# Performance work log

Hardware: AMD Instinct MI355X
Metric: run time of the kernel (lower is better)

## Reference

```python
import jax, jax.numpy as jnp
import numpy as np
from jax.scipy.special import logsumexp

B, L = 32, 128
NEG = -1e9
SPAN_LAMB = 0.5


def setup_inputs() -> dict:
    key = jax.random.key(0)
    ks = jax.random.split(key, 8)
    span_logits = jax.random.normal(ks[0], (B, L, L, 2), jnp.float32)
    ph = jax.random.normal(ks[1], (B, L, L), jnp.float32)
    pt = jax.random.normal(ks[2], (B, L, L), jnp.float32)
    ph_arc = jax.random.normal(ks[3], (B, L, L), jnp.float32)
    spans_ind = jax.random.randint(ks[4], (B, L, L), 0, 3, jnp.int32)
    ph_ind = jax.random.randint(ks[5], (B, L, L), 0, 2, jnp.int32)
    pt_ind = jax.random.randint(ks[6], (B, L, L), 0, 2, jnp.int32)
    lens = jax.random.randint(ks[7], (B,), L // 2, L + 1, jnp.int32)
    i = jnp.arange(L)
    # maskspan[b,i,j] = valid right-closed span i..j within sentence b; row 0 sums to lens
    maskspan = (i[None, :, None] <= i[None, None, :]) & (i[None, None, :] < lens[:, None, None])
    maskarc = (i[None, :, None] < lens[:, None, None]) & (i[None, None, :] < lens[:, None, None])
    return dict(span_logits=span_logits, ph=ph, pt=pt, ph_arc=ph_arc,
                spans_ind=spans_ind, ph_ind=ph_ind, pt_ind=pt_ind,
                maskspan=maskspan, maskarc=maskarc)


def _inside_logZ(span_logits, lens):
    # CYK inside algorithm over right-closed spans; returns sum_b logZ_b.
    scores = logsumexp(span_logits, axis=-1)  # [B,L,L] span score = lse over labels
    Ln = scores.shape[1]
    ar = jnp.arange(Ln)
    # width-0 base: s[i,i] = scores[i,i]
    s0 = jnp.where(jnp.eye(Ln, dtype=bool)[None], scores, NEG)
    li = ar[:, None] + ar[None, :]        # [L,L]: left child right end i+k
    ri = li + 1                           # right child left end i+k+1
    li_c = jnp.clip(li, 0, Ln - 1)
    ri_c = jnp.clip(ri, 0, Ln - 1)

    def step(s, w):
        j = ar + w
        jc = jnp.clip(j, 0, Ln - 1)
        left = s[:, ar[:, None], li_c]                 # [B,L,L] left[b,i,k]=s[b,i,i+k]
        right = s[:, ri_c, jc[:, None]]                # right[b,i,k]=s[b,i+k+1,i+w]
        comb = jnp.where(ar[None, None, :] < w, left + right, NEG)
        new = scores[:, ar, jc] + logsumexp(comb, axis=-1)  # [B,L]
        valid = (j < Ln)[None, :]
        cur = s[:, ar, jc]
        s = s.at[:, ar, jc].set(jnp.where(valid, new, cur))
        return s, None

    s, _ = jax.lax.scan(step, s0, jnp.arange(1, Ln))
    logZ = jnp.take_along_axis(s[:, 0, :], (lens - 1)[:, None], axis=1)[:, 0]
    return logZ.sum()


def _bce_mean(x, y, m):
    # stable BCEWithLogits, mean over masked elements
    l = jnp.maximum(x, 0.0) - x * y + jnp.log1p(jnp.exp(-jnp.abs(x)))
    return jnp.where(m, l, 0.0).sum() / m.sum().astype(jnp.float32)


def reference(span_logits, ph, pt, ph_arc, spans_ind, ph_ind, pt_ind, maskspan, maskarc):
    lens = maskspan[:, 0].sum(-1)                         # [B]
    spans_b = jnp.where(spans_ind > 0, spans_ind - 1, spans_ind).astype(bool)
    # label marginals = d logZ / d span_logits (matches torch autograd-based cyk)
    marginals = jax.grad(_inside_logZ)(span_logits, lens)  # [B,L,L,2]
    pos_mask = maskspan & spans_b
    neg_mask = maskspan & (~spans_b)
    pos_loss = jnp.log(jnp.where(pos_mask, jnp.maximum(marginals[..., 1], 1e-38), 1.0)).sum()
    neg_loss = jnp.log(jnp.where(neg_mask, jnp.maximum(marginals[..., 0], 1e-38), 1.0)).sum()
    loss_spans = -(pos_loss + neg_loss) / lens.sum().astype(jnp.float32)
    loss_ph = _bce_mean(ph, ph_ind.astype(jnp.float32), maskarc)
    loss_pt = _bce_mean(pt, pt_ind.astype(jnp.float32), maskarc)
    return SPAN_LAMB * loss_spans + (1.0 - SPAN_LAMB) * (loss_ph + loss_pt)
```

## Files before the change

kernel.cpp:

```cpp
#include <hip/hip_runtime.h>
#include <float.h>

#define NB 32
#define NBCE 32
#define L 128
#define NT 1024
#define R 132
#define PAD 8
#define LOGMIN -87.49823f

__device__ __forceinline__ int mask_mode(const void* p) {
    unsigned int v = ((const unsigned int*)p)[0];
    if (v == 1u) return 1;
    if (v == 0x3F800000u) return 2;
    return 0;
}
__device__ __forceinline__ bool mask_at(const void* p, int mode, int idx) {
    if (mode == 1) return ((const int*)p)[idx] != 0;
    if (mode == 2) return ((const float*)p)[idx] != 0.0f;
    return ((const unsigned char*)p)[idx] != 0;
}

__device__ __forceinline__ float lse2(float a, float b) {
    return fmaxf(a, b) + log1pf(__expf(-fabsf(a - b)));
}

template<int C>
__device__ __forceinline__ float dppf(float x) {
    return __int_as_float(__builtin_amdgcn_mov_dpp(__float_as_int(x), C, 0xF, 0xF, true));
}
template<int T>
__device__ __forceinline__ float bfly_max(float x) {
    x = fmaxf(x, dppf<0xB1>(x));
    x = fmaxf(x, dppf<0x4E>(x));
    x = fmaxf(x, dppf<0x141>(x));
    if (T == 16) x = fmaxf(x, dppf<0x140>(x));
    return x;
}
template<int T>
__device__ __forceinline__ float bfly_add(float x) {
    x += dppf<0xB1>(x);
    x += dppf<0x4E>(x);
    x += dppf<0x141>(x);
    if (T == 16) x += dppf<0x140>(x);
    return x;
}

template<int T, int M>
__device__ __forceinline__ void load_blk(float4* buf, int sub, int clo, int chi,
                                         const float* p1, const float* p2, float& mloc) {
    const int kb0 = clo >> 2;
#pragma unroll
    for (int m = 0; m < M; ++m) {
        const int c0 = (kb0 + sub + T * m) << 2;
        if (c0 >= chi) break;
        const float4 a = *(const float4*)(p1 + c0);
        const float4 b = *(const float4*)(p2 + c0);
        const unsigned rng = (unsigned)(chi - clo);
        float4 v;
        v.x = ((unsigned)(c0 + 0 - clo) < rng) ? a.x + b.x : -FLT_MAX;
        v.y = ((unsigned)(c0 + 1 - clo) < rng) ? a.y + b.y : -FLT_MAX;
        v.z = ((unsigned)(c0 + 2 - clo) < rng) ? a.z + b.z : -FLT_MAX;
        v.w = ((unsigned)(c0 + 3 - clo) < rng) ? a.w + b.w : -FLT_MAX;
        buf[m] = v;
        mloc = fmaxf(mloc, fmaxf(fmaxf(v.x, v.y), fmaxf(v.z, v.w)));
    }
}
template<int T, int M>
__device__ __forceinline__ void sumexp_blk(const float4* buf, int sub, int clo, int chi,
                                           float Mv, float& s) {
    const int kb0 = clo >> 2;
#pragma unroll
    for (int m = 0; m < M; ++m) {
        const int c0 = (kb0 + sub + T * m) << 2;
        if (c0 >= chi) break;
        const float4 v = buf[m];
        s += __expf(v.x - Mv) + __expf(v.y - Mv) + __expf(v.z - Mv) + __expf(v.w - Mv);
    }
}

__global__ __launch_bounds__(NT, 1) void tree_dp_kernel(
    const float* __restrict__ logits,
    const int*   __restrict__ spans_ind,
    const void*  __restrict__ maskspan,
    const float* __restrict__ ph, const float* __restrict__ pt,
    const int* __restrict__ ph_ind, const int* __restrict__ pt_ind,
    const void* __restrict__ maskarc,
    double*      __restrict__ ws)
{
    const int tid = threadIdx.x;

    if (blockIdx.x >= NB) {
        const int mode = mask_mode(maskarc);
        const int tot = NB * L * L;
        double sph = 0.0, spt = 0.0, cnt = 0.0;
        for (int idx = (blockIdx.x - NB) * NT + tid; idx < tot; idx += NBCE * NT) {
            if (mask_at(maskarc, mode, idx)) {
                float x = ph[idx]; float y = (float)ph_ind[idx];
                sph += (double)(fmaxf(x, 0.0f) - x * y + log1pf(__expf(-fabsf(x))));
                x = pt[idx]; y = (float)pt_ind[idx];
                spt += (double)(fmaxf(x, 0.0f) - x * y + log1pf(__expf(-fabsf(x))));
                cnt += 1.0;
            }
        }
        for (int off = 32; off > 0; off >>= 1) {
            sph += __shfl_down(sph, off);
            spt += __shfl_down(spt, off);
            cnt += __shfl_down(cnt, off);
        }
        if ((tid & 63) == 0) {
            atomicAdd(&ws[2], sph); atomicAdd(&ws[3], spt); atomicAdd(&ws[4], cnt);
        }
        return;
    }

    __shared__ __align__(16) float Am[L * R + PAD];
    __shared__ __align__(16) float Gm[L * R + PAD];

    const int b = blockIdx.x;
    const int mbase = b * L * L;
    const int mode = mask_mode(maskspan);

    int predv = (tid < L) && mask_at(maskspan, mode, mbase + tid);
    const int n = __syncthreads_count(predv);

    const float* lg = logits + (size_t)b * L * L * 2;
    const int* si = spans_ind + mbase;

    for (int e = tid; e < L * L; e += NT) {
        int ii = e >> 7, jj = e & (L - 1);
        if (ii <= jj && jj < n) {
            const float* p = lg + (size_t)e * 2;
            float v = lse2(p[0], p[1]);
            Am[ii * R + jj] = v;
            if (ii >= 1) Am[jj * R + ii - 1] = v;
            Gm[ii * R + jj] = v; Gm[jj * R + ii] = v;
        }
    }
    __syncthreads();

    for (int w = 1; w < n; ++w) {
        const int c = n - w;
        if (c > 64) {
            const int cell = tid >> 3, sub = tid & 7;
            if (cell < c) {
                const int i = cell, j = i + w;
                float4 buf[3]; float mloc = -FLT_MAX;
                load_blk<8, 3>(buf, sub, i, j, &Am[i * R], &Am[j * R], mloc);
                float Mv = bfly_max<8>(mloc);
                float s = 0.0f;
                sumexp_blk<8, 3>(buf, sub, i, j, Mv, s);
                float S = bfly_add<8>(s);
                if (sub == 0) {
                    float val = Am[i * R + j] + Mv + __logf(S);
                    Am[i * R + j] = val;
                    Am[j * R + i - 1] = val;
                }
            }
        } else {
            const int cell = tid >> 4, sub = tid & 15;
            if (cell < c) {
                const int i = cell, j = i + w;
                float4 buf[2]; float mloc = -FLT_MAX;
                load_blk<16, 2>(buf, sub, i, j, &Am[i * R], &Am[j * R], mloc);
                float Mv = bfly_max<16>(mloc);
                float s = 0.0f;
                sumexp_blk<16, 2>(buf, sub, i, j, Mv, s);
                float S = bfly_add<16>(s);
                if (sub == 0) {
                    float val = Am[i * R + j] + Mv + __logf(S);
                    Am[i * R + j] = val;
                    Am[j * R + i - 1] = val;
                }
            }
        }
        __syncthreads();
    }

    const float logZ = Am[n - 1];

    {
        float tmp[16];
#pragma unroll
        for (int p = 0; p < 16; ++p) {
            const int e = tid + p * NT;
            const int r = e >> 7, cc = e & (L - 1);
            tmp[p] = 0.0f;
            if (cc < r && r < n)
                tmp[p] = (cc == 0) ? Am[r] : Am[r * R + cc - 1];
        }
        __syncthreads();
#pragma unroll
        for (int p = 0; p < 16; ++p) {
            const int e = tid + p * NT;
            const int r = e >> 7, cc = e & (L - 1);
            if (cc < r && r < n) Am[r * R + cc] = tmp[p];
        }
    }
    __syncthreads();

    for (int w = n - 2; w >= 1; --w) {
        const int c = n - w;
        if (c > 64) {
            const int cell = tid >> 3, sub = tid & 7;
            if (cell < c) {
                const int i = cell, j = i + w;
                float4 b1[4], b2[4]; float mloc = -FLT_MAX;
                load_blk<8, 4>(b1, sub, j + 1, n, &Gm[i * R], &Am[(j + 1) * R], mloc);
                const float* pa2 = &Am[(i >= 1 ? i - 1 : 0) * R];
                load_blk<8, 4>(b2, sub, 0, i, &Gm[j * R], pa2, mloc);
                float Mv = bfly_max<8>(mloc);
                float s = 0.0f;
                sumexp_blk<8, 4>(b1, sub, j + 1, n, Mv, s);
                sumexp_blk<8, 4>(b2, sub, 0, i, Mv, s);
                float S = bfly_add<8>(s);
                if (sub == 0) {
                    float val = Gm[i * R + j] + Mv + __logf(S);
                    Gm[i * R + j] = val; Gm[j * R + i] = val;
                }
            }
        } else {
            const int cell = tid >> 4, sub = tid & 15;
            if (cell < c) {
                const int i = cell, j = i + w;
                float4 b1[2], b2[1]; float mloc = -FLT_MAX;
                load_blk<16, 2>(b1, sub, j + 1, n, &Gm[i * R], &Am[(j + 1) * R], mloc);
                const float* pa2 = &Am[(i >= 1 ? i - 1 : 0) * R];
                load_blk<16, 1>(b2, sub, 0, i, &Gm[j * R], pa2, mloc);
                float Mv = bfly_max<16>(mloc);
                float s = 0.0f;
                sumexp_blk<16, 2>(b1, sub, j + 1, n, Mv, s);
                sumexp_blk<16, 1>(b2, sub, 0, i, Mv, s);
                float S = bfly_add<16>(s);
                if (sub == 0) {
                    float val = Gm[i * R + j] + Mv + __logf(S);
                    Gm[i * R + j] = val; Gm[j * R + i] = val;
                }
            }
        }
        __syncthreads();
    }

    double local = 0.0;
    {
        const int cell = tid >> 3, sub = tid & 7;
        if (cell < n) {
            const int i = cell;
            float4 b1[4], b2[4]; float mloc = -FLT_MAX;
            const float* pa1 = &Am[(i + 1 < n ? i + 1 : 0) * R];
            load_blk<8, 4>(b1, sub, i + 1, n, &Gm[i * R], pa1, mloc);
            const float* pa2 = &Am[(i >= 1 ? i - 1 : 0) * R];
            load_blk<8, 4>(b2, sub, 0, i, &Gm[i * R], pa2, mloc);
            float Mv = bfly_max<8>(mloc);
            float s = 0.0f;
            sumexp_blk<8, 4>(b1, sub, i + 1, n, Mv, s);
            sumexp_blk<8, 4>(b2, sub, 0, i, Mv, s);
            float S = bfly_add<8>(s);
            if (sub == 0) {
                float beta_ii = Mv + __logf(S);
                const float* p = lg + ((size_t)i * L + i) * 2;
                float lc = (si[i * L + i] == 2) ? p[1] : p[0];
                local += (double)fmaxf(beta_ii - logZ + lc, LOGMIN);
            }
        }
    }

    for (int e = tid; e < L * L; e += NT) {
        int ii = e >> 7, jj = e & (L - 1);
        if (ii < jj && jj < n) {
            const float* p = lg + (size_t)e * 2;
            float a = p[0], cc = p[1];
            float sc = lse2(a, cc);
            float lc = (si[e] == 2) ? cc : a;
            float logm = Am[ii * R + jj] + Gm[ii * R + jj] - logZ + lc - 2.0f * sc;
            local += (double)fmaxf(logm, LOGMIN);
        }
    }

    for (int off = 32; off > 0; off >>= 1)
        local += __shfl_down(local, off);
    if ((tid & 63) == 0) atomicAdd(&ws[0], local);
    if (tid == 0) atomicAdd(&ws[1], (double)n);
}

__global__ void finalize_kernel(const double* __restrict__ ws, float* __restrict__ out) {
    double loss_spans = -ws[0] / ws[1];
    double bce = (ws[2] + ws[3]) / ws[4];
    out[0] = (float)(0.5 * loss_spans + 0.5 * bce);
}

extern "C" void kernel_launch(void* const* d_in, const int* in_sizes, int n_in,
                              void* d_out, int out_size, void* d_ws, size_t ws_size,
                              hipStream_t stream) {
    (void)in_sizes; (void)n_in; (void)out_size; (void)ws_size;
    const float* span_logits = (const float*)d_in[0];
    const float* ph          = (const float*)d_in[1];
    const float* pt          = (const float*)d_in[2];
    const int*   spans_ind   = (const int*)d_in[4];
    const int*   ph_ind      = (const int*)d_in[5];
    const int*   pt_ind      = (const int*)d_in[6];
    const void*  maskspan    = d_in[7];
    const void*  maskarc     = d_in[8];
    double* ws = (double*)d_ws;
    float* out = (float*)d_out;

    hipMemsetAsync(d_ws, 0, 5 * sizeof(double), stream);
    hipLaunchKernelGGL(tree_dp_kernel, dim3(NB + NBCE), dim3(NT), 0, stream,
                       span_logits, spans_ind, maskspan,
                       ph, pt, ph_ind, pt_ind, maskarc, ws);
    hipLaunchKernelGGL(finalize_kernel, dim3(1), dim3(1), 0, stream, ws, out);
}
```

Measured before the change: 343.6 us.

## Block inside/outside CYK passes into 8-width chunks with register-level wavefront updates

Replaces the one-barrier-per-width inside and outside DP loops with chunks of eight widths. Each chunk first computes a bulk partial logsumexp (max, sum) for every cell from already-finished spans, cooperatively across the block into a shared P buffer. Three wavefronts then finish the dependent in-chunk terms in registers, using shuffles and online-merge logsumexp. This cuts the number of __syncthreads by roughly 8x and removes the 16-thread-per-cell path, at the cost of much more intricate index logic and extra per-chunk serial work on three wavefronts.

```diff
diff --git a/kernel.cpp b/kernel.cpp
--- a/kernel.cpp
+++ b/kernel.cpp
@@ -29,20 +29,16 @@
 __device__ __forceinline__ float dppf(float x) {
     return __int_as_float(__builtin_amdgcn_mov_dpp(__float_as_int(x), C, 0xF, 0xF, true));
 }
-template<int T>
-__device__ __forceinline__ float bfly_max(float x) {
+__device__ __forceinline__ float bfly_max8(float x) {
     x = fmaxf(x, dppf<0xB1>(x));
     x = fmaxf(x, dppf<0x4E>(x));
     x = fmaxf(x, dppf<0x141>(x));
-    if (T == 16) x = fmaxf(x, dppf<0x140>(x));
     return x;
 }
-template<int T>
-__device__ __forceinline__ float bfly_add(float x) {
+__device__ __forceinline__ float bfly_add8(float x) {
     x += dppf<0xB1>(x);
     x += dppf<0x4E>(x);
     x += dppf<0x141>(x);
-    if (T == 16) x += dppf<0x140>(x);
     return x;
 }
 
@@ -79,6 +75,18 @@
     }
 }
 
+__device__ __forceinline__ void omerge(float t, float& m, float& s) {
+    float nm = fmaxf(m, t);
+    s = s * __expf(m - nm) + __expf(t - nm);
+    m = nm;
+}
+__device__ __forceinline__ void omerge_mask(float t, bool mk, float& m, float& s) {
+    float tm = mk ? t : -FLT_MAX;
+    float nm = fmaxf(m, tm);
+    s = s * __expf(m - nm) + (mk ? __expf(t - nm) : 0.0f);
+    m = nm;
+}
+
 __global__ __launch_bounds__(NT, 1) void tree_dp_kernel(
     const float* __restrict__ logits,
     const int*   __restrict__ spans_ind,
@@ -116,6 +124,7 @@
 
     __shared__ __align__(16) float Am[L * R + PAD];
     __shared__ __align__(16) float Gm[L * R + PAD];
+    __shared__ float2 P[8][128];
 
     const int b = blockIdx.x;
     const int mbase = b * L * L;
@@ -139,38 +148,97 @@
     }
     __syncthreads();
 
-    for (int w = 1; w < n; ++w) {
-        const int c = n - w;
-        if (c > 64) {
-            const int cell = tid >> 3, sub = tid & 7;
-            if (cell < c) {
-                const int i = cell, j = i + w;
-                float4 buf[3]; float mloc = -FLT_MAX;
-                load_blk<8, 3>(buf, sub, i, j, &Am[i * R], &Am[j * R], mloc);
-                float Mv = bfly_max<8>(mloc);
-                float s = 0.0f;
-                sumexp_blk<8, 3>(buf, sub, i, j, Mv, s);
-                float S = bfly_add<8>(s);
-                if (sub == 0) {
-                    float val = Am[i * R + j] + Mv + __logf(S);
-                    Am[i * R + j] = val;
-                    Am[j * R + i - 1] = val;
-                }
-            }
-        } else {
-            const int cell = tid >> 4, sub = tid & 15;
-            if (cell < c) {
-                const int i = cell, j = i + w;
-                float4 buf[2]; float mloc = -FLT_MAX;
-                load_blk<16, 2>(buf, sub, i, j, &Am[i * R], &Am[j * R], mloc);
-                float Mv = bfly_max<16>(mloc);
-                float s = 0.0f;
-                sumexp_blk<16, 2>(buf, sub, i, j, Mv, s);
-                float S = bfly_add<16>(s);
-                if (sub == 0) {
-                    float val = Am[i * R + j] + Mv + __logf(S);
-                    Am[i * R + j] = val;
-                    Am[j * R + i - 1] = val;
+    const int wv = tid >> 6;
+    const int ln = tid & 63;
+    const int bcell = wv * 56 + ln;
+    const int ic = min(bcell, L - 1);
+    const bool ownIn  = (wv < 2) ? (ln < 56) : (ln < 16);
+    const bool ownOut = (wv == 0) ? true : (ln >= 8 && ln < ((wv == 1) ? 64 : 16));
+    float llo[7];
+    float vlo[8];
+
+    if (wv < 3) {
+        float r[8];
+        const float ld0 = Am[ic * R + ic];
+#pragma unroll
+        for (int d = 0; d < 8; ++d) {
+            const int w = d + 1;
+            const bool valid = (bcell + w < n);
+            const int jcl = min(bcell + w, L - 1);
+            const float dsc = Am[jcl * R + jcl];
+            const float scij = Gm[ic * R + jcl];
+            float m = -FLT_MAX, s = 0.0f;
+#pragma unroll
+            for (int e = 0; e < 8; ++e) {
+                if (e < w) {
+                    const int f = w - 1 - e;
+                    float lv = (e == 0) ? ld0 : r[e - 1];
+                    float rv = (f == 0) ? dsc : __shfl_down(r[f - 1], e + 1);
+                    omerge(lv + rv, m, s);
+                }
+            }
+            float val = scij + m + __logf(s);
+            r[d] = val;
+            if (valid && ownIn) {
+                Am[bcell * R + bcell + w] = val;
+                Am[(bcell + w) * R + bcell - 1] = val;
+            }
+        }
+        llo[0] = ld0;
+#pragma unroll
+        for (int e = 1; e < 7; ++e)
+            llo[e] = r[e - 1];
+    }
+    __syncthreads();
+
+    for (int w0 = 9; w0 < n; w0 += 8) {
+        {
+            const int cellA = tid >> 3, sub = tid & 7;
+#pragma unroll
+            for (int d = 0; d < 8; ++d) {
+                const int w = w0 + d;
+                if (w < n && cellA < n - w) {
+                    const int i = cellA, j = i + w;
+                    float4 buf[4]; float mloc = -FLT_MAX;
+                    load_blk<8, 4>(buf, sub, i + d, i + w0, &Am[i * R], &Am[j * R], mloc);
+                    float Mv = bfly_max8(mloc);
+                    float s = 0.0f;
+                    sumexp_blk<8, 4>(buf, sub, i + d, i + w0, Mv, s);
+                    float S = bfly_add8(s);
+                    if (sub == 0) P[d][i] = make_float2(Mv, S);
+                }
+            }
+        }
+        __syncthreads();
+        if (wv < 3) {
+            float r[8];
+#pragma unroll
+            for (int d = 0; d < 8; ++d) {
+                const int w = w0 + d;
+                const bool valid = (w < n) && (bcell + w < n);
+                const int jcl = min(bcell + w, L - 1);
+                float2 pp = P[d][ic];
+                float m = pp.x, s = pp.y;
+#pragma unroll
+                for (int e = 0; e < 7; ++e) {
+                    if (e < d) {
+                        float rv = __shfl_down(r[d - 1 - e], e + 1);
+                        omerge(llo[e] + rv, m, s);
+                    }
+                }
+#pragma unroll
+                for (int h = 0; h < 7; ++h) {
+                    if (h < d) {
+                        float rv = Am[jcl * R + min(ic + w0 + h, L - 1)];
+                        omerge(r[h] + rv, m, s);
+                    }
+                }
+                float scij = Gm[ic * R + jcl];
+                float val = scij + m + __logf(s);
+                r[d] = val;
+                if (valid && ownIn) {
+                    Am[bcell * R + bcell + w] = val;
+                    Am[(bcell + w) * R + bcell - 1] = val;
                 }
             }
         }
@@ -184,57 +252,99 @@
 #pragma unroll
         for (int p = 0; p < 16; ++p) {
             const int e = tid + p * NT;
-            const int r = e >> 7, cc = e & (L - 1);
+            const int rr = e >> 7, cc = e & (L - 1);
             tmp[p] = 0.0f;
-            if (cc < r && r < n)
-                tmp[p] = (cc == 0) ? Am[r] : Am[r * R + cc - 1];
+            if (cc < rr && rr < n)
+                tmp[p] = (cc == 0) ? Am[rr] : Am[rr * R + cc - 1];
         }
         __syncthreads();
 #pragma unroll
         for (int p = 0; p < 16; ++p) {
             const int e = tid + p * NT;
-            const int r = e >> 7, cc = e & (L - 1);
-            if (cc < r && r < n) Am[r * R + cc] = tmp[p];
+            const int rr = e >> 7, cc = e & (L - 1);
+            if (cc < rr && rr < n) Am[rr * R + cc] = tmp[p];
         }
     }
     __syncthreads();
 
-    for (int w = n - 2; w >= 1; --w) {
-        const int c = n - w;
-        if (c > 64) {
-            const int cell = tid >> 3, sub = tid & 7;
-            if (cell < c) {
-                const int i = cell, j = i + w;
-                float4 b1[4], b2[4]; float mloc = -FLT_MAX;
-                load_blk<8, 4>(b1, sub, j + 1, n, &Gm[i * R], &Am[(j + 1) * R], mloc);
-                const float* pa2 = &Am[(i >= 1 ? i - 1 : 0) * R];
-                load_blk<8, 4>(b2, sub, 0, i, &Gm[j * R], pa2, mloc);
-                float Mv = bfly_max<8>(mloc);
-                float s = 0.0f;
-                sumexp_blk<8, 4>(b1, sub, j + 1, n, Mv, s);
-                sumexp_blk<8, 4>(b2, sub, 0, i, Mv, s);
-                float S = bfly_add<8>(s);
-                if (sub == 0) {
-                    float val = Gm[i * R + j] + Mv + __logf(S);
-                    Gm[i * R + j] = val; Gm[j * R + i] = val;
-                }
-            }
-        } else {
-            const int cell = tid >> 4, sub = tid & 15;
-            if (cell < c) {
-                const int i = cell, j = i + w;
-                float4 b1[2], b2[1]; float mloc = -FLT_MAX;
-                load_blk<16, 2>(b1, sub, j + 1, n, &Gm[i * R], &Am[(j + 1) * R], mloc);
-                const float* pa2 = &Am[(i >= 1 ? i - 1 : 0) * R];
-                load_blk<16, 1>(b2, sub, 0, i, &Gm[j * R], pa2, mloc);
-                float Mv = bfly_max<16>(mloc);
-                float s = 0.0f;
-                sumexp_blk<16, 2>(b1, sub, j + 1, n, Mv, s);
-                sumexp_blk<16, 1>(b2, sub, 0, i, Mv, s);
-                float S = bfly_add<16>(s);
-                if (sub == 0) {
-                    float val = Gm[i * R + j] + Mv + __logf(S);
-                    Gm[i * R + j] = val; Gm[j * R + i] = val;
+    if (wv < 3) {
+        const int im1 = max(ic - 1, 0);
+#pragma unroll
+        for (int v = 1; v < 8; ++v)
+            vlo[v] = Am[im1 * R + max(ic - v, 0)];
+    }
+
+    const int bTop = 1 + 8 * ((n - 3) >> 3);
+    for (int b0 = bTop; b0 >= 1; b0 -= 8) {
+        float scg[8];
+        if (wv < 3) {
+#pragma unroll
+            for (int d = 0; d < 8; ++d)
+                scg[d] = Gm[ic * R + min(ic + b0 + d, L - 1)];
+        }
+        {
+            const int cellA = tid >> 3, sub = tid & 7;
+#pragma unroll
+            for (int d = 0; d < 8; ++d) {
+                const int w = b0 + d;
+                if (w <= n - 2 && cellA < n - w) {
+                    const int i = cellA, j = i + w;
+                    float mloc = -FLT_MAX;
+                    float4 b1[4], b2[4];
+                    const int clo1 = j + (8 - d);
+                    const bool h1 = clo1 < n;
+                    if (h1) load_blk<8, 4>(b1, sub, clo1, n, &Gm[i * R], &Am[(j + 1) * R], mloc);
+                    const int chi2 = i + d - 7;
+                    const bool h2 = chi2 > 0;
+                    if (h2) load_blk<8, 4>(b2, sub, 0, chi2, &Gm[j * R], &Am[(i - 1) * R], mloc);
+                    float Mv = bfly_max8(mloc);
+                    float s = 0.0f;
+                    if (h1) sumexp_blk<8, 4>(b1, sub, clo1, n, Mv, s);
+                    if (h2) sumexp_blk<8, 4>(b2, sub, 0, chi2, Mv, s);
+                    float S = bfly_add8(s);
+                    if (sub == 0) P[d][i] = make_float2(Mv, S);
+                }
+            }
+        }
+        __syncthreads();
+        if (wv < 3) {
+            float r[8];
+#pragma unroll
+            for (int dd = 0; dd < 8; ++dd) {
+                const int d = 7 - dd;
+                const int w = b0 + d;
+                const bool valid = (w <= n - 2) && (bcell + w < n);
+                const int j = bcell + w;
+                const int jcl = min(j, L - 1);
+                const int jp1 = min(j + 1, L - 1);
+                float2 pp = P[d][ic];
+                float m = pp.x, s = pp.y;
+#pragma unroll
+                for (int u = 1; u < 8; ++u) {
+                    if (u < 8 - d) {
+                        const bool mk = valid && (j + u < n);
+                        float g = (w + u < n - 1) ? r[d + u] : Gm[ic * R + min(j + u, L - 1)];
+                        float a = Am[jp1 * R + min(j + u, L - 1)];
+                        omerge_mask(g + a, mk, m, s);
+                    }
+                }
+#pragma unroll
+                for (int v = 1; v < 8; ++v) {
+                    if (v < 8 - d) {
+                        float g;
+                        if (w + v < n - 1)
+                            g = __shfl_up(r[d + v], v);
+                        else
+                            g = Gm[jcl * R + max(bcell - v, 0)];
+                        const bool mk = valid && (bcell - v >= 0);
+                        omerge_mask(g + vlo[v], mk, m, s);
+                    }
+                }
+                float val = scg[d] + m + __logf(s);
+                r[d] = val;
+                if (valid && ownOut) {
+                    Gm[bcell * R + j] = val;
+                    Gm[j * R + bcell] = val;
                 }
             }
         }
@@ -250,12 +360,12 @@
             const float* pa1 = &Am[(i + 1 < n ? i + 1 : 0) * R];
             load_blk<8, 4>(b1, sub, i + 1, n, &Gm[i * R], pa1, mloc);
             const float* pa2 = &Am[(i >= 1 ? i - 1 : 0) * R];
-            load_blk<8, 4>(b2, sub, 0, i, &Gm[i * R], pa2, mloc);
-            float Mv = bfly_max<8>(mloc);
+            if (i > 0) load_blk<8, 4>(b2, sub, 0, i, &Gm[i * R], pa2, mloc);
+            float Mv = bfly_max8(mloc);
             float s = 0.0f;
             sumexp_blk<8, 4>(b1, sub, i + 1, n, Mv, s);
-            sumexp_blk<8, 4>(b2, sub, 0, i, Mv, s);
-            float S = bfly_add<8>(s);
+            if (i > 0) sumexp_blk<8, 4>(b2, sub, 0, i, Mv, s);
+            float S = bfly_add8(s);
             if (sub == 0) {
                 float beta_ii = Mv + __logf(S);
                 const float* p = lg + ((size_t)i * L + i) * 2;
```

Measured after the change: 420.0 us. 22.2% more time.

## Process two DP diagonals per barrier using wave shuffles and LDS flags

Applied to the files above, without the earlier changes.

The inside and outside CYK sweeps now handle two span widths per __syncthreads. The second width's log-sum-exp is computed from the terms already available and then merged online with the two terms that depend on the first width. Those neighbour values come through wave shuffles, or through a workgroup-scope acquire/release flag spin-wait when the neighbour cell sits in another wavefront. Storage also changes: Am is kept symmetric instead of shifted, loads switch from float4 to scalar strided reads, and the padding grows. The aim is to halve the number of block-wide barriers on the serial critical path, at the cost of spin-waits, scalar LDS loads and a more complex dependency scheme.

```diff
diff --git a/kernel.cpp b/kernel.cpp
--- a/kernel.cpp
+++ b/kernel.cpp
@@ -6,7 +6,7 @@
 #define L 128
 #define NT 1024
 #define R 132
-#define PAD 8
+#define PAD 40
 #define LOGMIN -87.49823f
 
 __device__ __forceinline__ int mask_mode(const void* p) {
@@ -46,36 +46,153 @@
     return x;
 }
 
-template<int T, int M>
-__device__ __forceinline__ void load_blk(float4* buf, int sub, int clo, int chi,
-                                         const float* p1, const float* p2, float& mloc) {
-    const int kb0 = clo >> 2;
+template<int T, int NU>
+__device__ __forceinline__ void load_terms(float* v, int sub, int nterm,
+                                           const float* p1, const float* p2, float& mloc) {
+    p1 += sub; p2 += sub;
 #pragma unroll
-    for (int m = 0; m < M; ++m) {
-        const int c0 = (kb0 + sub + T * m) << 2;
-        if (c0 >= chi) break;
-        const float4 a = *(const float4*)(p1 + c0);
-        const float4 b = *(const float4*)(p2 + c0);
-        const unsigned rng = (unsigned)(chi - clo);
-        float4 v;
-        v.x = ((unsigned)(c0 + 0 - clo) < rng) ? a.x + b.x : -FLT_MAX;
-        v.y = ((unsigned)(c0 + 1 - clo) < rng) ? a.y + b.y : -FLT_MAX;
-        v.z = ((unsigned)(c0 + 2 - clo) < rng) ? a.z + b.z : -FLT_MAX;
-        v.w = ((unsigned)(c0 + 3 - clo) < rng) ? a.w + b.w : -FLT_MAX;
-        buf[m] = v;
-        mloc = fmaxf(mloc, fmaxf(fmaxf(v.x, v.y), fmaxf(v.z, v.w)));
-    }
-}
-template<int T, int M>
-__device__ __forceinline__ void sumexp_blk(const float4* buf, int sub, int clo, int chi,
-                                           float Mv, float& s) {
-    const int kb0 = clo >> 2;
+    for (int m = 0; m < NU; ++m) {
+        if (m * T >= nterm) break;
+        float a = p1[m * T] + p2[m * T];
+        a = (sub + m * T < nterm) ? a : -FLT_MAX;
+        v[m] = a;
+        mloc = fmaxf(mloc, a);
+    }
+}
+template<int T, int NU>
+__device__ __forceinline__ void sum_exp(const float* v, int nterm, float M, float& s) {
 #pragma unroll
-    for (int m = 0; m < M; ++m) {
-        const int c0 = (kb0 + sub + T * m) << 2;
-        if (c0 >= chi) break;
-        const float4 v = buf[m];
-        s += __expf(v.x - Mv) + __expf(v.y - Mv) + __expf(v.z - Mv) + __expf(v.w - Mv);
+    for (int m = 0; m < NU; ++m) {
+        if (m * T >= nterm) break;
+        s += __expf(v[m] - M);
+    }
+}
+
+template<int T, int NU>
+__device__ __forceinline__ void lse_part1(const float* p1, const float* p2, int nt,
+                                          int sub, float& M, float& S) {
+    float v[NU]; float mloc = -FLT_MAX;
+    load_terms<T, NU>(v, sub, nt, p1, p2, mloc);
+    float Mv = bfly_max<T>(mloc);
+    float s = 0.0f;
+    sum_exp<T, NU>(v, nt, Mv, s);
+    S = bfly_add<T>(s);
+    M = Mv;
+}
+template<int T, int NU1, int NU2>
+__device__ __forceinline__ void lse_part2(const float* a1, const float* a2, int nt1,
+                                          const float* b1, const float* b2, int nt2,
+                                          int sub, float& M, float& S) {
+    float v1[NU1]; float v2[NU2]; float mloc = -FLT_MAX;
+    load_terms<T, NU1>(v1, sub, nt1, a1, a2, mloc);
+    load_terms<T, NU2>(v2, sub, nt2, b1, b2, mloc);
+    float Mv = bfly_max<T>(mloc);
+    float s = 0.0f;
+    sum_exp<T, NU1>(v1, nt1, Mv, s);
+    sum_exp<T, NU2>(v2, nt2, Mv, s);
+    S = bfly_add<T>(s);
+    M = Mv;
+}
+
+__device__ __forceinline__ void omerge(float t, float& m, float& s) {
+    float nm = fmaxf(m, t);
+    s = s * __expf(m - nm) + __expf(t - nm);
+    m = nm;
+}
+__device__ __forceinline__ void omerge_mask(float t, bool mk, float& m, float& s) {
+    float tm = mk ? t : -FLT_MAX;
+    float nm = fmaxf(m, tm);
+    s = s * __expf(m - nm) + (mk ? __expf(t - nm) : 0.0f);
+    m = nm;
+}
+
+__device__ __forceinline__ void pub(int* f, int ep) {
+    __hip_atomic_store(f, ep, __ATOMIC_RELEASE, __HIP_MEMORY_SCOPE_WORKGROUP);
+}
+__device__ __forceinline__ void waitflag(int* f, int ep) {
+    while (__hip_atomic_load(f, __ATOMIC_ACQUIRE, __HIP_MEMORY_SCOPE_WORKGROUP) < ep) {}
+}
+
+template<int T>
+__device__ __forceinline__ void inside_pair(float* Am, int* flag, int n, int w, int tid) {
+    const int i = tid / T, sub = tid % T;
+    const int c = n - w;
+    const int j = i + w, j2 = j + 1;
+    const bool act1 = (i < c);
+    const bool act2 = (w + 1 < n) && (i < c - 1);
+    float val1 = -FLT_MAX;
+    if (act1) {
+        float M, S;
+        lse_part1<T, 8>(&Am[i * R + i], &Am[j * R + i + 1], w, sub, M, S);
+        val1 = Am[i * R + j] + M + __logf(S);
+        if (sub == 0) {
+            Am[i * R + j] = val1;
+            Am[j * R + i] = val1;
+            pub(&flag[i], w);
+        }
+    }
+    float M2 = -FLT_MAX, S2 = 0.0f;
+    if (act2)
+        lse_part1<T, 8>(&Am[i * R + i + 1], &Am[j2 * R + i + 2], w - 1, sub, M2, S2);
+    float sh = __shfl_down(val1, T);
+    if (act2) {
+        float nb;
+        if ((i & (64 / T - 1)) == (64 / T - 1)) {
+            waitflag(&flag[i + 1], w);
+            nb = Am[(i + 1) * R + j2];
+        } else nb = sh;
+        float m = M2, s = S2;
+        omerge(val1 + Am[j2 * R + j2], m, s);
+        omerge(Am[i * R + i] + nb, m, s);
+        float val2 = Am[i * R + j2] + m + __logf(s);
+        if (sub == 0) { Am[i * R + j2] = val2; Am[j2 * R + i] = val2; }
+    }
+}
+
+template<int T, int NU>
+__device__ __forceinline__ void outside_pair(const float* Am, float* Gm, int* flag,
+                                             int n, int w, int ep, int tid) {
+    const int i = tid / T, sub = tid % T;
+    const int c = n - w;
+    const int j = i + w, jp = j - 1;
+    const bool act1 = (i < c);
+    const bool act2 = (w >= 2) && (i <= c);
+    float val1 = -FLT_MAX;
+    if (act1) {
+        float M, S;
+        const float* av = &Am[(i >= 1 ? i - 1 : 0) * R];
+        lse_part2<T, NU, NU>(&Gm[i * R + j + 1], &Am[(j + 1) * R + j + 1], n - 1 - j,
+                             &Gm[j * R], av, i, sub, M, S);
+        val1 = Gm[i * R + j] + M + __logf(S);
+        if (sub == 0) {
+            Gm[i * R + j] = val1;
+            Gm[j * R + i] = val1;
+            pub(&flag[i], ep);
+        }
+    }
+    float M2 = -FLT_MAX, S2 = 0.0f;
+    if (act2) {
+        const float* av = &Am[(i >= 1 ? i - 1 : 0) * R];
+        const int jcl = min(j, n - 1);
+        lse_part2<T, NU, NU>(&Gm[i * R + j + 1], &Am[jcl * R + j + 1], n - j - 1,
+                             &Gm[jp * R], av, i - 1, sub, M2, S2);
+    }
+    float sh = __shfl_up(val1, T);
+    if (act2) {
+        float nb = sh;
+        if ((i & (64 / T - 1)) == 0) {
+            if (i >= 1) {
+                waitflag(&flag[i - 1], ep);
+                nb = Gm[(i - 1) * R + jp];
+            }
+        }
+        float m = M2, s = S2;
+        const int jd = min(j, n - 1);
+        omerge_mask(val1 + Am[jd * R + jd], i + w < n, m, s);
+        const int id = (i >= 1) ? i - 1 : 0;
+        omerge_mask(nb + Am[id * R + id], i >= 1, m, s);
+        float val2 = Gm[i * R + jp] + m + __logf(s);
+        if (sub == 0) { Gm[i * R + jp] = val2; Gm[jp * R + i] = val2; }
     }
 }
 
@@ -116,6 +233,7 @@
 
     __shared__ __align__(16) float Am[L * R + PAD];
     __shared__ __align__(16) float Gm[L * R + PAD];
+    __shared__ int flag[128];
 
     const int b = blockIdx.x;
     const int mbase = b * L * L;
@@ -127,137 +245,44 @@
     const float* lg = logits + (size_t)b * L * L * 2;
     const int* si = spans_ind + mbase;
 
+    if (tid < 128) flag[tid] = 0;
     for (int e = tid; e < L * L; e += NT) {
         int ii = e >> 7, jj = e & (L - 1);
         if (ii <= jj && jj < n) {
             const float* p = lg + (size_t)e * 2;
             float v = lse2(p[0], p[1]);
-            Am[ii * R + jj] = v;
-            if (ii >= 1) Am[jj * R + ii - 1] = v;
+            Am[ii * R + jj] = v; Am[jj * R + ii] = v;
             Gm[ii * R + jj] = v; Gm[jj * R + ii] = v;
         }
     }
     __syncthreads();
 
-    for (int w = 1; w < n; ++w) {
-        const int c = n - w;
-        if (c > 64) {
-            const int cell = tid >> 3, sub = tid & 7;
-            if (cell < c) {
-                const int i = cell, j = i + w;
-                float4 buf[3]; float mloc = -FLT_MAX;
-                load_blk<8, 3>(buf, sub, i, j, &Am[i * R], &Am[j * R], mloc);
-                float Mv = bfly_max<8>(mloc);
-                float s = 0.0f;
-                sumexp_blk<8, 3>(buf, sub, i, j, Mv, s);
-                float S = bfly_add<8>(s);
-                if (sub == 0) {
-                    float val = Am[i * R + j] + Mv + __logf(S);
-                    Am[i * R + j] = val;
-                    Am[j * R + i - 1] = val;
-                }
-            }
-        } else {
-            const int cell = tid >> 4, sub = tid & 15;
-            if (cell < c) {
-                const int i = cell, j = i + w;
-                float4 buf[2]; float mloc = -FLT_MAX;
-                load_blk<16, 2>(buf, sub, i, j, &Am[i * R], &Am[j * R], mloc);
-                float Mv = bfly_max<16>(mloc);
-                float s = 0.0f;
-                sumexp_blk<16, 2>(buf, sub, i, j, Mv, s);
-                float S = bfly_add<16>(s);
-                if (sub == 0) {
-                    float val = Am[i * R + j] + Mv + __logf(S);
-                    Am[i * R + j] = val;
-                    Am[j * R + i - 1] = val;
-                }
-            }
-        }
+    for (int w = 1; w < n; w += 2) {
+        if (n - w > 64) inside_pair<8>(Am, flag, n, w, tid);
+        else            inside_pair<16>(Am, flag, n, w, tid);
         __syncthreads();
     }
 
     const float logZ = Am[n - 1];
 
-    {
-        float tmp[16];
-#pragma unroll
-        for (int p = 0; p < 16; ++p) {
-            const int e = tid + p * NT;
-            const int r = e >> 7, cc = e & (L - 1);
-            tmp[p] = 0.0f;
-            if (cc < r && r < n)
-                tmp[p] = (cc == 0) ? Am[r] : Am[r * R + cc - 1];
-        }
-        __syncthreads();
-#pragma unroll
-        for (int p = 0; p < 16; ++p) {
-            const int e = tid + p * NT;
-            const int r = e >> 7, cc = e & (L - 1);
-            if (cc < r && r < n) Am[r * R + cc] = tmp[p];
-        }
-    }
-    __syncthreads();
-
-    for (int w = n - 2; w >= 1; --w) {
-        const int c = n - w;
-        if (c > 64) {
-            const int cell = tid >> 3, sub = tid & 7;
-            if (cell < c) {
-                const int i = cell, j = i + w;
-                float4 b1[4], b2[4]; float mloc = -FLT_MAX;
-                load_blk<8, 4>(b1, sub, j + 1, n, &Gm[i * R], &Am[(j + 1) * R], mloc);
-                const float* pa2 = &Am[(i >= 1 ? i - 1 : 0) * R];
-                load_blk<8, 4>(b2, sub, 0, i, &Gm[j * R], pa2, mloc);
-                float Mv = bfly_max<8>(mloc);
-                float s = 0.0f;
-                sumexp_blk<8, 4>(b1, sub, j + 1, n, Mv, s);
-                sumexp_blk<8, 4>(b2, sub, 0, i, Mv, s);
-                float S = bfly_add<8>(s);
-                if (sub == 0) {
-                    float val = Gm[i * R + j] + Mv + __logf(S);
-                    Gm[i * R + j] = val; Gm[j * R + i] = val;
-                }
-            }
-        } else {
-            const int cell = tid >> 4, sub = tid & 15;
-            if (cell < c) {
-                const int i = cell, j = i + w;
-                float4 b1[2], b2[1]; float mloc = -FLT_MAX;
-                load_blk<16, 2>(b1, sub, j + 1, n, &Gm[i * R], &Am[(j + 1) * R], mloc);
-                const float* pa2 = &Am[(i >= 1 ? i - 1 : 0) * R];
-                load_blk<16, 1>(b2, sub, 0, i, &Gm[j * R], pa2, mloc);
-                float Mv = bfly_max<16>(mloc);
-                float s = 0.0f;
-                sumexp_blk<16, 2>(b1, sub, j + 1, n, Mv, s);
-                sumexp_blk<16, 1>(b2, sub, 0, i, Mv, s);
-                float S = bfly_add<16>(s);
-                if (sub == 0) {
-                    float val = Gm[i * R + j] + Mv + __logf(S);
-                    Gm[i * R + j] = val; Gm[j * R + i] = val;
-                }
-            }
-        }
+    for (int w = n - 2; w >= 1; w -= 2) {
+        const int ep = 2 * n - w;
+        if (n - w + 1 > 64) outside_pair<8, 16>(Am, Gm, flag, n, w, ep, tid);
+        else                outside_pair<16, 4>(Am, Gm, flag, n, w, ep, tid);
         __syncthreads();
     }
 
     double local = 0.0;
     {
-        const int cell = tid >> 3, sub = tid & 7;
-        if (cell < n) {
-            const int i = cell;
-            float4 b1[4], b2[4]; float mloc = -FLT_MAX;
+        const int i = tid >> 3, sub = tid & 7;
+        if (i < n) {
+            float M, S;
             const float* pa1 = &Am[(i + 1 < n ? i + 1 : 0) * R];
-            load_blk<8, 4>(b1, sub, i + 1, n, &Gm[i * R], pa1, mloc);
             const float* pa2 = &Am[(i >= 1 ? i - 1 : 0) * R];
-            load_blk<8, 4>(b2, sub, 0, i, &Gm[i * R], pa2, mloc);
-            float Mv = bfly_max<8>(mloc);
-            float s = 0.0f;
-            sumexp_blk<8, 4>(b1, sub, i + 1, n, Mv, s);
-            sumexp_blk<8, 4>(b2, sub, 0, i, Mv, s);
-            float S = bfly_add<8>(s);
+            lse_part2<8, 16, 16>(&Gm[i * R + i + 1], pa1 + i + 1, n - 1 - i,
+                                 &Gm[i * R], pa2, i, sub, M, S);
             if (sub == 0) {
-                float beta_ii = Mv + __logf(S);
+                float beta_ii = M + __logf(S);
                 const float* p = lg + ((size_t)i * L + i) * 2;
                 float lc = (si[i * L + i] == 2) ? p[1] : p[0];
                 local += (double)fmaxf(beta_ii - logZ + lc, LOGMIN);
```

Result: slower. 439.0 us (+27.8%).
